# Performance work log

Measured on AMD Instinct MI355X. Metric: run time of the kernel, lower is better.

## Reference

```python
import jax, jax.numpy as jnp
import numpy as np

N, E = 50000, 300000
IN, FC, AC, H, C1, C2, OUT = 1024, 128, 20, 4, 10, 5, 3
FCN = FC + AC + H * C2  # 168


def bn_eval(x, g, b):
    # BatchNorm1d in eval mode with running_mean=0, running_var=1
    return x * (g / jnp.sqrt(1.0 + 1e-5)) + b


def add_self_loops(edge_index, edge_attr, n):
    # PyG add_self_loops with fill_value='mean': self-loop attr = mean of incoming edge attrs
    src, dst = edge_index[0], edge_index[1]
    ones = jnp.ones(src.shape[0], jnp.float32)
    deg = jax.ops.segment_sum(ones, dst, num_segments=n)
    mean_attr = jax.ops.segment_sum(edge_attr, dst, num_segments=n) / jnp.maximum(deg, 1.0)[:, None]
    loop = jnp.arange(n, dtype=src.dtype)
    return (jnp.concatenate([src, loop]), jnp.concatenate([dst, loop]),
            jnp.concatenate([edge_attr, mean_attr], 0))


def gatv2(x, src, dst, eattr, Wl, bl, Wr, br, We, att, b, n):
    # GATv2Conv (concat=True, negative_slope=0.2, edge_dim=1)
    h, c = att.shape
    xl = (x @ Wl + bl).reshape(n, h, c)
    xr = (x @ Wr + br).reshape(n, h, c)
    em = (eattr @ We).reshape(-1, h, c)
    m = jax.nn.leaky_relu(xl[src] + xr[dst] + em, 0.2)   # [E', H, C]
    logit = jnp.einsum('ehc,hc->eh', m, att)              # [E', H]
    mx = jax.ops.segment_max(logit, dst, num_segments=n)
    ex = jnp.exp(logit - mx[dst])
    den = jax.ops.segment_sum(ex, dst, num_segments=n)
    alpha = ex / (den[dst] + 1e-16)                       # segment softmax over dst
    out = jax.ops.segment_sum(xl[src] * alpha[..., None], dst, num_segments=n)
    return out.reshape(n, h * c) + b


def setup_inputs() -> dict:
    key = jax.random.key(0)
    ks = jax.random.split(key, 24)
    rn = lambda k, s: jax.random.normal(k, s, jnp.float32) * 0.05
    return {
        'features': jax.random.normal(ks[0], (N, IN), jnp.float32),
        'edges': jax.random.randint(ks[1], (2, E), 0, N),
        'edges2': jax.random.randint(ks[2], (2, E), 0, N),
        'edge_features': jax.random.normal(ks[3], (E, 1), jnp.float32),
        'additional_features': jax.random.normal(ks[4], (N, AC), jnp.float32),
        'sage_Wl': rn(ks[5], (IN, FC)), 'sage_bl': jnp.zeros((FC,), jnp.float32),
        'sage_Wr': rn(ks[6], (IN, FC)),
        'g1_Wl': rn(ks[7], (AC, H * C1)), 'g1_bl': jnp.zeros((H * C1,), jnp.float32),
        'g1_Wr': rn(ks[8], (AC, H * C1)), 'g1_br': jnp.zeros((H * C1,), jnp.float32),
        'g1_We': rn(ks[9], (1, H * C1)), 'g1_att': rn(ks[10], (H, C1)),
        'g1_b': jnp.zeros((H * C1,), jnp.float32),
        'g2_Wl': rn(ks[11], (H * C1, H * C2)), 'g2_bl': jnp.zeros((H * C2,), jnp.float32),
        'g2_Wr': rn(ks[12], (H * C1, H * C2)), 'g2_br': jnp.zeros((H * C2,), jnp.float32),
        'g2_We': rn(ks[13], (1, H * C2)), 'g2_att': rn(ks[14], (H, C2)),
        'g2_b': jnp.zeros((H * C2,), jnp.float32),
        'fc1_W': rn(ks[15], (FCN, FCN)), 'fc1_b': jnp.zeros((FCN,), jnp.float32),
        'fc2_W': rn(ks[16], (FCN, OUT)), 'fc2_b': jnp.zeros((OUT,), jnp.float32),
        'bnx_g': jnp.ones((FC,), jnp.float32), 'bnx_b': jnp.zeros((FC,), jnp.float32),
        'bny_g': jnp.ones((H * C2,), jnp.float32), 'bny_b': jnp.zeros((H * C2,), jnp.float32),
        'bnf_g': jnp.ones((FCN,), jnp.float32), 'bnf_b': jnp.zeros((FCN,), jnp.float32),
    }


def reference(features, edges, edges2, edge_features, additional_features,
              sage_Wl, sage_bl, sage_Wr,
              g1_Wl, g1_bl, g1_Wr, g1_br, g1_We, g1_att, g1_b,
              g2_Wl, g2_bl, g2_Wr, g2_br, g2_We, g2_att, g2_b,
              fc1_W, fc1_b, fc2_W, fc2_b,
              bnx_g, bnx_b, bny_g, bny_b, bnf_g, bnf_b):
    n = features.shape[0]
    # --- SAGEConv (mean aggr): out = lin_l(mean_j x_j) + lin_r(x_i) ---
    src, dst = edges[0], edges[1]
    deg = jax.ops.segment_sum(jnp.ones(src.shape[0], jnp.float32), dst, num_segments=n)
    aggr = jax.ops.segment_sum(features[src], dst, num_segments=n) / jnp.maximum(deg, 1.0)[:, None]
    x = aggr @ sage_Wl + sage_bl + features @ sage_Wr
    x = bn_eval(x, bnx_g, bnx_b)
    # --- GATv2 stack (self loops with mean edge-attr fill) ---
    s2, d2, ea = add_self_loops(edges2, edge_features, n)
    y = gatv2(additional_features, s2, d2, ea, g1_Wl, g1_bl, g1_Wr, g1_br, g1_We, g1_att, g1_b, n)
    y = jax.nn.leaky_relu(y, 0.01)  # activation (dropout off in eval)
    y = gatv2(y, s2, d2, ea, g2_Wl, g2_bl, g2_Wr, g2_br, g2_We, g2_att, g2_b, n)
    y = bn_eval(y, bny_g, bny_b)
    # --- MLP head ---
    z = jax.nn.leaky_relu(jnp.concatenate([x, y], axis=1), 0.01)
    z = jnp.concatenate([z, additional_features], axis=1) @ fc1_W + fc1_b
    z = jax.nn.relu(bn_eval(z, bnf_g, bnf_b))
    return z @ fc2_W + fc2_b
```

## Files before the change

### kernel.cpp

```cpp
#include <hip/hip_runtime.h>
#include <hip/hip_bf16.h>
#include <cfloat>

__device__ __forceinline__ float lrelu(float x, float a) { return x > 0.0f ? x : a * x; }

__device__ __forceinline__ unsigned short f2bf(float f) {
    unsigned u = __float_as_uint(f);
    unsigned r = (u + 0x7FFFu + ((u >> 16) & 1u)) >> 16;
    return (unsigned short)r;
}
__device__ __forceinline__ float bf2f(unsigned short u) {
    return __uint_as_float((unsigned)u << 16);
}

typedef __attribute__((ext_vector_type(8))) short short8;
typedef __attribute__((ext_vector_type(4))) float f32x4;

#define BN_RSQ 0.99999500003749968750f
#define SCAN_B 256

__global__ void zero_ws(uint4* __restrict__ p, int n16)
{
    int t = blockIdx.x * blockDim.x + threadIdx.x;
    if (t < n16) p[t] = make_uint4(0u, 0u, 0u, 0u);
}

__global__ void prep_all(const float* __restrict__ sWl, const float* __restrict__ sWr,
                         unsigned short* __restrict__ Btp,
                         const float* __restrict__ fc1W, unsigned short* __restrict__ Bt1p,
                         const float* __restrict__ g1Wl, const float* __restrict__ g1Wr,
                         unsigned short* __restrict__ Bg1,
                         const float* __restrict__ g2Wl, const float* __restrict__ g2Wr,
                         unsigned short* __restrict__ Bg2,
                         const int* __restrict__ e1d, const int* __restrict__ e2d,
                         const float* __restrict__ ef,
                         int* __restrict__ cnt1, int* __restrict__ cnt2,
                         float* __restrict__ easum, int E)
{
    int idx = blockIdx.x * blockDim.x + threadIdx.x;
    if (idx < 262144) {
        int j = idx & 7, lane = (idx >> 3) & 63, fn = (idx >> 9) & 3, wid = (idx >> 11) & 3, t = idx >> 13;
        int c = wid * 64 + fn * 16 + (lane & 15);
        int k = t * 32 + (lane >> 4) * 8 + j;
        float v = (c < 128) ? sWl[(size_t)k * 128 + c] : sWr[(size_t)k * 128 + (c - 128)];
        Btp[idx] = f2bf(v);
        return;
    }
    idx -= 262144;
    if (idx < 36864) {
        int j = idx & 7, lane = (idx >> 3) & 63, fn = (idx >> 9) & 3, q = idx >> 11;
        int wid = q % 3, t = q / 3;
        int c = wid * 64 + fn * 16 + (lane & 15);
        int k = t * 32 + (lane >> 4) * 8 + j;
        float v = (c < 168 && k < 168) ? fc1W[(size_t)k * 168 + c] : 0.0f;
        Bt1p[idx] = f2bf(v);
        return;
    }
    idx -= 36864;
    if (idx < 2560) {
        int j = idx & 7, lane = (idx >> 3) & 63, fn = idx >> 9;
        int c = fn * 16 + (lane & 15);
        int k = (lane >> 4) * 8 + j;
        float v = 0.0f;
        if (k < 20) v = (c < 40) ? g1Wl[(size_t)k * 40 + c] : g1Wr[(size_t)k * 40 + (c - 40)];
        Bg1[idx] = f2bf(v);
        return;
    }
    idx -= 2560;
    if (idx < 3072) {
        int j = idx & 7, lane = (idx >> 3) & 63, q = idx >> 9;
        int fn = q % 3, t = q / 3;
        int c = fn * 16 + (lane & 15);
        int k = t * 32 + (lane >> 4) * 8 + j;
        float v = 0.0f;
        if (k < 40 && c < 40) v = (c < 20) ? g2Wl[(size_t)k * 20 + c] : g2Wr[(size_t)k * 20 + (c - 20)];
        Bg2[idx] = f2bf(v);
        return;
    }
    idx -= 3072;
    if (idx < E) {
        atomicAdd(&cnt1[e1d[idx]], 1);
        int d2 = e2d[idx];
        atomicAdd(&cnt2[d2], 1);
        atomicAdd(&easum[d2], ef[idx]);
    }
}

__global__ void scan1(const int* __restrict__ cnt1, const int* __restrict__ cnt2,
                      int* __restrict__ off1, int* __restrict__ off2,
                      int* __restrict__ bsum1, int* __restrict__ bsum2, int M)
{
    __shared__ int sh[SCAN_B];
    int y = blockIdx.y;
    const int* cnt = y ? cnt2 : cnt1;
    int* excl = y ? off2 : off1;
    int* bsum = y ? bsum2 : bsum1;
    int i = blockIdx.x * SCAN_B + threadIdx.x;
    int v = (i < M) ? cnt[i] + y : 0;
    sh[threadIdx.x] = v;
    __syncthreads();
    for (int o = 1; o < SCAN_B; o <<= 1) {
        int t = (threadIdx.x >= o) ? sh[threadIdx.x - o] : 0;
        __syncthreads();
        sh[threadIdx.x] += t;
        __syncthreads();
    }
    if (i < M) excl[i] = sh[threadIdx.x] - v;
    if (threadIdx.x == SCAN_B - 1) bsum[blockIdx.x] = sh[threadIdx.x];
}

__global__ void scan2(int* __restrict__ bsum1, int* __restrict__ bsum2, int nb)
{
    __shared__ int sh[SCAN_B];
    int* bsum = blockIdx.y ? bsum2 : bsum1;
    int v = ((int)threadIdx.x < nb) ? bsum[threadIdx.x] : 0;
    sh[threadIdx.x] = v;
    __syncthreads();
    for (int o = 1; o < SCAN_B; o <<= 1) {
        int t = (threadIdx.x >= o) ? sh[threadIdx.x - o] : 0;
        __syncthreads();
        sh[threadIdx.x] += t;
        __syncthreads();
    }
    if ((int)threadIdx.x < nb) bsum[threadIdx.x] = sh[threadIdx.x] - v;
}

__global__ void scan3(int* __restrict__ off1, int* __restrict__ off2,
                      const int* __restrict__ bsum1, const int* __restrict__ bsum2,
                      const int* __restrict__ cnt1, const int* __restrict__ cnt2,
                      const float* __restrict__ easum, float* __restrict__ ealoop, int M)
{
    int y = blockIdx.y;
    int* off = y ? off2 : off1;
    const int* bsum = y ? bsum2 : bsum1;
    const int* cnt = y ? cnt2 : cnt1;
    int i = blockIdx.x * SCAN_B + threadIdx.x;
    if (i < M) {
        int v = off[i] + bsum[blockIdx.x];
        off[i] = v;
        if (i == M - 1) off[M] = v + cnt[i] + y;
        if (y) ealoop[i] = easum[i] / fmaxf((float)cnt2[i], 1.0f);
    }
}

__global__ __launch_bounds__(256) void stageA(
    const float* __restrict__ A, const unsigned short* __restrict__ Btp,
    unsigned short* __restrict__ P,
    const int* __restrict__ e1s, const int* __restrict__ e1d,
    const int* __restrict__ e2s, const int* __restrict__ e2d,
    const float* __restrict__ ef, const float* __restrict__ ealoop,
    const int* __restrict__ off1, const int* __restrict__ off2,
    int* __restrict__ cnt1, int* __restrict__ cnt2,
    int* __restrict__ srcs1, int2* __restrict__ se2,
    const float* __restrict__ addf, const unsigned short* __restrict__ Bg1,
    const float* __restrict__ g1bl, const float* __restrict__ g1br,
    unsigned short* __restrict__ xl1b, unsigned short* __restrict__ xr1b,
    int M, int E, int Eext, int Gg, int Gf)
{
    __shared__ __align__(16) char smem[20480];
    const int bid = blockIdx.x;
    const int tid = threadIdx.x;

    if (bid < Gg) {
        typedef unsigned short As2_t[64][72];
        As2_t* As2 = reinterpret_cast<As2_t*>(smem);
        const int wid = tid >> 6, lane = tid & 63;
        const int m0 = bid * 64;
        const int l16 = lane & 15, g = lane >> 4;
        const int colbase = wid * 64 + l16;
        const short8* Bv = reinterpret_cast<const short8*>(Btp);
        const int srow = tid >> 4, scol = (tid & 15) * 4;

        f32x4 acc[4][4] = {};
        float4 rcur[4], rnext[4];

#pragma unroll
        for (int p = 0; p < 4; ++p) {
            int ar = m0 + p * 16 + srow;
            rcur[p] = make_float4(0.f, 0.f, 0.f, 0.f);
            if (ar < M) rcur[p] = *reinterpret_cast<const float4*>(&A[(size_t)ar * 1024 + scol]);
        }
#pragma unroll
        for (int p = 0; p < 4; ++p) {
            ushort4 u;
            u.x = f2bf(rcur[p].x); u.y = f2bf(rcur[p].y); u.z = f2bf(rcur[p].z); u.w = f2bf(rcur[p].w);
            *reinterpret_cast<ushort4*>(&As2[0][p * 16 + srow][scol]) = u;
        }
#pragma unroll
        for (int p = 0; p < 4; ++p) {
            int ar = m0 + p * 16 + srow;
            rcur[p] = make_float4(0.f, 0.f, 0.f, 0.f);
            if (ar < M) rcur[p] = *reinterpret_cast<const float4*>(&A[(size_t)ar * 1024 + 64 + scol]);
        }
        __syncthreads();

        for (int c = 0; c < 16; ++c) {
            const int buf = c & 1;
            if (c < 14) {
                const int k0 = (c + 2) * 64;
#pragma unroll
                for (int p = 0; p < 4; ++p) {
                    int ar = m0 + p * 16 + srow;
                    rnext[p] = make_float4(0.f, 0.f, 0.f, 0.f);
                    if (ar < M) rnext[p] = *reinterpret_cast<const float4*>(&A[(size_t)ar * 1024 + k0 + scol]);
                }
            }
#pragma unroll
            for (int t = 0; t < 2; ++t) {
                const int ks = c * 2 + t;
                short8 afr[4], bfr[4];
#pragma unroll
                for (int fm = 0; fm < 4; ++fm)
                    afr[fm] = *reinterpret_cast<const short8*>(&As2[buf][fm * 16 + l16][t * 32 + g * 8]);
#pragma unroll
                for (int fn = 0; fn < 4; ++fn)
                    bfr[fn] = Bv[((ks * 4 + wid) * 4 + fn) * 64 + lane];
#pragma unroll
                for (int fm = 0; fm < 4; ++fm)
#pragma unroll
                    for (int fn = 0; fn < 4; ++fn)
                        acc[fm][fn] = __builtin_amdgcn_mfma_f32_16x16x32_bf16(
                            afr[fm], bfr[fn], acc[fm][fn], 0, 0, 0);
            }
            if (c < 15) {
#pragma unroll
                for (int p = 0; p < 4; ++p) {
                    ushort4 u;
                    u.x = f2bf(rcur[p].x); u.y = f2bf(rcur[p].y);
                    u.z = f2bf(rcur[p].z); u.w = f2bf(rcur[p].w);
                    *reinterpret_cast<ushort4*>(&As2[buf ^ 1][p * 16 + srow][scol]) = u;
                }
            }
            __syncthreads();
#pragma unroll
            for (int p = 0; p < 4; ++p) rcur[p] = rnext[p];
        }

#pragma unroll
        for (int fm = 0; fm < 4; ++fm) {
#pragma unroll
            for (int r = 0; r < 4; ++r) {
                int row = m0 + fm * 16 + g * 4 + r;
                if (row < M) {
#pragma unroll
                    for (int fn = 0; fn < 4; ++fn)
                        P[(size_t)row * 256 + colbase + fn * 16] = f2bf(acc[fm][fn][r]);
                }
            }
        }
    } else if (bid < Gg + Gf) {
        int t = (bid - Gg) * 256 + tid;
        if (t < E) {
            int d = e1d[t];
            int pos = atomicSub(&cnt1[d], 1) - 1;
            srcs1[off1[d] + pos] = e1s[t];
        }
        int t2 = t - E;
        if (t2 >= 0 && t2 < Eext) {
            if (t2 < E) {
                int d = e2d[t2];
                int pos = atomicSub(&cnt2[d], 1) - 1;
                se2[off2[d] + pos] = make_int2(e2s[t2], __float_as_int(ef[t2]));
            } else {
                int nn = t2 - E;
                se2[off2[nn + 1] - 1] = make_int2(nn, __float_as_int(ealoop[nn]));
            }
        }
    } else {
        const int wid = tid >> 6, lane = tid & 63;
        const int tile = (bid - Gg - Gf) * 4 + wid;
        const int m0 = tile * 64;
        if (m0 >= M) return;
        unsigned short (*xs)[40] = reinterpret_cast<unsigned short(*)[40]>(smem + wid * 5120);
        const int l16 = lane & 15, g = lane >> 4;
        const short8* Bv = reinterpret_cast<const short8*>(Bg1);

#pragma unroll
        for (int i = 0; i < 5; ++i) {
            int q = i * 64 + lane;
            int f = q * 4;
            int row = f / 20, col = f % 20;
            int ar = m0 + row;
            float4 v = make_float4(0.f, 0.f, 0.f, 0.f);
            if (ar < M) v = *reinterpret_cast<const float4*>(&addf[(size_t)ar * 20 + col]);
            ushort4 u;
            u.x = f2bf(v.x); u.y = f2bf(v.y); u.z = f2bf(v.z); u.w = f2bf(v.w);
            *reinterpret_cast<ushort4*>(&xs[row][col]) = u;
        }
        ushort4 zz; zz.x = 0; zz.y = 0; zz.z = 0; zz.w = 0;
#pragma unroll
        for (int c = 20; c < 32; c += 4)
            *reinterpret_cast<ushort4*>(&xs[lane][c]) = zz;

        f32x4 acc[4][5] = {};
        short8 afr[4], bfr[5];
#pragma unroll
        for (int fm = 0; fm < 4; ++fm)
            afr[fm] = *reinterpret_cast<const short8*>(&xs[fm * 16 + l16][g * 8]);
#pragma unroll
        for (int fn = 0; fn < 5; ++fn)
            bfr[fn] = Bv[fn * 64 + lane];
#pragma unroll
        for (int fm = 0; fm < 4; ++fm)
#pragma unroll
            for (int fn = 0; fn < 5; ++fn)
                acc[fm][fn] = __builtin_amdgcn_mfma_f32_16x16x32_bf16(
                    afr[fm], bfr[fn], acc[fm][fn], 0, 0, 0);

#pragma unroll
        for (int fm = 0; fm < 4; ++fm) {
#pragma unroll
            for (int r = 0; r < 4; ++r) {
                int row = m0 + fm * 16 + g * 4 + r;
                if (row < M) {
#pragma unroll
                    for (int fn = 0; fn < 5; ++fn) {
                        int col = fn * 16 + l16;
                        float v = acc[fm][fn][r];
                        if (col < 40) {
                            int h = col / 10, c = col % 10;
                            xl1b[((size_t)row * 4 + h) * 16 + c] = f2bf(v + g1bl[col]);
                        } else if (col < 80) {
                            int cc = col - 40, h = cc / 10, c = cc % 10;
                            xr1b[((size_t)row * 4 + h) * 16 + c] = f2bf(v + g1br[cc]);
                        }
                    }
                }
            }
        }
    }
}

template <int H, int C, int BPAD, int MODE>
__device__ __forceinline__ void gat_node_core(
    const int2* __restrict__ se2, const int* __restrict__ off2,
    const unsigned short* __restrict__ xlb, const unsigned short* __restrict__ xrb,
    const float* __restrict__ We, const float* __restrict__ att,
    const float* __restrict__ b,
    const float* __restrict__ bng, const float* __restrict__ bnb,
    void* __restrict__ outv, int n, int h)
{
    float xrc[C], atth[C], weh[C];
    {
        short8 sv[BPAD / 8];
#pragma unroll
        for (int q = 0; q < BPAD / 8; ++q)
            sv[q] = *reinterpret_cast<const short8*>(&xrb[((size_t)n * H + h) * BPAD + q * 8]);
#pragma unroll
        for (int c = 0; c < C; ++c) xrc[c] = bf2f((unsigned short)sv[c / 8][c % 8]);
    }
#pragma unroll
    for (int c = 0; c < C; ++c) {
        atth[c] = att[h * C + c];
        weh[c]  = We[h * C + c];
    }

    const int beg = off2[n], end = off2[n + 1];
    float mx = -FLT_MAX, den = 0.0f;
    float accv[C] = {};
    for (int j = beg; j < end; ++j) {
        int2 se = se2[j];
        int s = se.x;
        float ea = __int_as_float(se.y);
        short8 sv[BPAD / 8];
#pragma unroll
        for (int q = 0; q < BPAD / 8; ++q)
            sv[q] = *reinterpret_cast<const short8*>(&xlb[((size_t)s * H + h) * BPAD + q * 8]);
        float xv[C];
        float lg = 0.0f;
#pragma unroll
        for (int c = 0; c < C; ++c) {
            xv[c] = bf2f((unsigned short)sv[c / 8][c % 8]);
            float m = xv[c] + xrc[c] + ea * weh[c];
            lg += lrelu(m, 0.2f) * atth[c];
        }
        if (lg > mx) {
            float sc = __expf(mx - lg);
            den *= sc;
#pragma unroll
            for (int c = 0; c < C; ++c) accv[c] *= sc;
            mx = lg;
        }
        float ex = __expf(lg - mx);
        den += ex;
#pragma unroll
        for (int c = 0; c < C; ++c) accv[c] += ex * xv[c];
    }
    float inv = 1.0f / (den + 1e-16f);

#pragma unroll
    for (int c = 0; c < C; ++c) {
        int jch = h * C + c;
        float v = accv[c] * inv + b[jch];
        if (MODE == 1) {
            ((float*)outv)[(size_t)n * (H * C) + jch] = lrelu(v, 0.01f);
        } else {
            v = v * (bng[jch] * BN_RSQ) + bnb[jch];
            ((unsigned short*)outv)[(size_t)n * 168 + 128 + jch] = f2bf(lrelu(v, 0.01f));
        }
    }
}

__global__ void stageB(const int* __restrict__ srcs1, const int* __restrict__ off1,
                       const unsigned short* __restrict__ P, const float* __restrict__ bl,
                       const float* __restrict__ bng, const float* __restrict__ bnb,
                       unsigned short* __restrict__ z,
                       const int2* __restrict__ se2, const int* __restrict__ off2,
                       const unsigned short* __restrict__ xl1b, const unsigned short* __restrict__ xr1b,
                       const float* __restrict__ g1We, const float* __restrict__ g1att,
                       const float* __restrict__ g1b, float* __restrict__ y1,
                       int N, int Gg)
{
    const int bid = blockIdx.x;
    if (bid < Gg) {
        int t = bid * 256 + threadIdx.x;
        if (t >= N * 16) return;
        int n = t >> 4, g = t & 15;
        int beg = off1[n], end = off1[n + 1];
        float a[8] = {};
        for (int j = beg; j < end; ++j) {
            int s = srcs1[j];
            short8 v = *reinterpret_cast<const short8*>(&P[(size_t)s * 256 + g * 8]);
#pragma unroll
            for (int k = 0; k < 8; ++k) a[k] += bf2f((unsigned short)v[k]);
        }
        float inv = 1.0f / fmaxf((float)(end - beg), 1.0f);
        short8 pr = *reinterpret_cast<const short8*>(&P[(size_t)n * 256 + 128 + g * 8]);
        short8 zo;
#pragma unroll
        for (int k = 0; k < 8; ++k) {
            int cc = g * 8 + k;
            float x = a[k] * inv + bl[cc] + bf2f((unsigned short)pr[k]);
            x = x * (bng[cc] * BN_RSQ) + bnb[cc];
            zo[k] = (short)f2bf(lrelu(x, 0.01f));
        }
        *reinterpret_cast<short8*>(&z[(size_t)n * 168 + g * 8]) = zo;
    } else {
        int t = (bid - Gg) * 256 + threadIdx.x;
        if (t >= N * 4) return;
        gat_node_core<4, 10, 16, 1>(se2, off2, xl1b, xr1b, g1We, g1att, g1b,
                                    nullptr, nullptr, (void*)y1, t >> 2, t & 3);
    }
}

__global__ __launch_bounds__(64) void gat_lin2_mfma(
    const float* __restrict__ X, const unsigned short* __restrict__ Bp,
    const float* __restrict__ bl, const float* __restrict__ br,
    unsigned short* __restrict__ xlb, unsigned short* __restrict__ xrb, int M)
{
    __shared__ unsigned short xs[64][72];
    const int lane = threadIdx.x;
    const int m0 = blockIdx.x * 64;
    const int l16 = lane & 15, g = lane >> 4;
    const short8* Bv = reinterpret_cast<const short8*>(Bp);

#pragma unroll
    for (int i = 0; i < 10; ++i) {
        int q = i * 64 + lane;
        int f = q * 4;
        int row = f / 40, col = f % 40;
        int ar = m0 + row;
        float4 v = make_float4(0.f, 0.f, 0.f, 0.f);
        if (ar < M) v = *reinterpret_cast<const float4*>(&X[(size_t)ar * 40 + col]);
        ushort4 u;
        u.x = f2bf(v.x); u.y = f2bf(v.y); u.z = f2bf(v.z); u.w = f2bf(v.w);
        *reinterpret_cast<ushort4*>(&xs[row][col]) = u;
    }
    ushort4 zz; zz.x = 0; zz.y = 0; zz.z = 0; zz.w = 0;
#pragma unroll
    for (int c = 40; c < 64; c += 4)
        *reinterpret_cast<ushort4*>(&xs[lane][c]) = zz;

    f32x4 acc[4][3] = {};
#pragma unroll
    for (int t = 0; t < 2; ++t) {
        short8 afr[4], bfr[3];
#pragma unroll
        for (int fm = 0; fm < 4; ++fm)
            afr[fm] = *reinterpret_cast<const short8*>(&xs[fm * 16 + l16][t * 32 + g * 8]);
#pragma unroll
        for (int fn = 0; fn < 3; ++fn)
            bfr[fn] = Bv[(t * 3 + fn) * 64 + lane];
#pragma unroll
        for (int fm = 0; fm < 4; ++fm)
#pragma unroll
            for (int fn = 0; fn < 3; ++fn)
                acc[fm][fn] = __builtin_amdgcn_mfma_f32_16x16x32_bf16(
                    afr[fm], bfr[fn], acc[fm][fn], 0, 0, 0);
    }

#pragma unroll
    for (int fm = 0; fm < 4; ++fm) {
#pragma unroll
        for (int r = 0; r < 4; ++r) {
            int row = m0 + fm * 16 + g * 4 + r;
            if (row < M) {
#pragma unroll
                for (int fn = 0; fn < 3; ++fn) {
                    int col = fn * 16 + l16;
                    float v = acc[fm][fn][r];
                    if (col < 20) {
                        int h = col / 5, c = col % 5;
                        xlb[((size_t)row * 4 + h) * 8 + c] = f2bf(v + bl[col]);
                    } else if (col < 40) {
                        int cc = col - 20, h = cc / 5, c = cc % 5;
                        xrb[((size_t)row * 4 + h) * 8 + c] = f2bf(v + br[cc]);
                    }
                }
            }
        }
    }
}

__global__ void gat_node2(const int2* __restrict__ se2, const int* __restrict__ off2,
                          const unsigned short* __restrict__ xlb, const unsigned short* __restrict__ xrb,
                          const float* __restrict__ We, const float* __restrict__ att,
                          const float* __restrict__ b,
                          const float* __restrict__ bng, const float* __restrict__ bnb,
                          unsigned short* __restrict__ z, int N)
{
    int t = blockIdx.x * blockDim.x + threadIdx.x;
    if (t >= N * 4) return;
    gat_node_core<4, 5, 8, 2>(se2, off2, xlb, xrb, We, att, b, bng, bnb, (void*)z, t >> 2, t & 3);
}

__global__ __launch_bounds__(256) void mlp_mfma(
    const unsigned short* __restrict__ z, const float* __restrict__ addf,
    const unsigned short* __restrict__ Bt1p,
    const float* __restrict__ fc1b, const float* __restrict__ bnfg, const float* __restrict__ bnfb,
    const float* __restrict__ fc2W, const float* __restrict__ fc2b,
    float* __restrict__ out, int M)
{
    __shared__ __align__(16) char smem[64 * 169 * 4];
    unsigned short (*zs)[200] = reinterpret_cast<unsigned short(*)[200]>(smem);
    float (*ts)[169] = reinterpret_cast<float(*)[169]>(smem);
    const int tid = threadIdx.x;
    const int wid = tid >> 6, lane = tid & 63;
    const int m0 = blockIdx.x * 64;
    const int l16 = lane & 15, g = lane >> 4;
    const short8* Bv = reinterpret_cast<const short8*>(Bt1p);

#pragma unroll
    for (int p = 0; p < 13; ++p) {
        int idx = p * 256 + tid;
        if (idx < 3200) {
            int row = idx / 50, c4 = (idx % 50) * 4;
            int ar = m0 + row;
            ushort4 u; u.x = 0; u.y = 0; u.z = 0; u.w = 0;
            if (ar < M) {
                if (c4 < 148) {
                    u = *reinterpret_cast<const ushort4*>(&z[(size_t)ar * 168 + c4]);
                } else if (c4 < 168) {
                    float4 v = *reinterpret_cast<const float4*>(&addf[(size_t)ar * 20 + (c4 - 148)]);
                    u.x = f2bf(v.x); u.y = f2bf(v.y); u.z = f2bf(v.z); u.w = f2bf(v.w);
                }
            }
            *reinterpret_cast<ushort4*>(&zs[row][c4]) = u;
        }
    }
    __syncthreads();

    f32x4 acc[4][4] = {};
    if (wid < 3) {
#pragma unroll
        for (int t = 0; t < 6; ++t) {
            short8 afr[4], bfr[4];
#pragma unroll
            for (int fm = 0; fm < 4; ++fm)
                afr[fm] = *reinterpret_cast<const short8*>(&zs[fm * 16 + l16][t * 32 + g * 8]);
#pragma unroll
            for (int fn = 0; fn < 4; ++fn)
                bfr[fn] = Bv[((t * 3 + wid) * 4 + fn) * 64 + lane];
#pragma unroll
            for (int fm = 0; fm < 4; ++fm)
#pragma unroll
                for (int fn = 0; fn < 4; ++fn)
                    acc[fm][fn] = __builtin_amdgcn_mfma_f32_16x16x32_bf16(
                        afr[fm], bfr[fn], acc[fm][fn], 0, 0, 0);
        }
    }
    __syncthreads();
    if (wid < 3) {
        const int colbase = wid * 64 + l16;
#pragma unroll
        for (int fm = 0; fm < 4; ++fm) {
#pragma unroll
            for (int r = 0; r < 4; ++r) {
                int rr = fm * 16 + g * 4 + r;
#pragma unroll
                for (int fn = 0; fn < 4; ++fn) {
                    int col = colbase + fn * 16;
                    if (col < 168) {
                        float v = acc[fm][fn][r] + fc1b[col];
                        v = v * (bnfg[col] * BN_RSQ) + bnfb[col];
                        ts[rr][col] = fmaxf(v, 0.0f);
                    }
                }
            }
        }
    }
    __syncthreads();
    if (tid < 192) {
        int r = tid & 63, c = tid >> 6;
        float acc2 = fc2b[c];
#pragma unroll 4
        for (int k = 0; k < 168; ++k) acc2 += ts[r][k] * fc2W[k * 3 + c];
        int row = m0 + r;
        if (row < M) out[(size_t)row * 3 + c] = acc2;
    }
}

extern "C" void kernel_launch(void* const* d_in, const int* in_sizes, int n_in,
                              void* d_out, int out_size, void* d_ws, size_t ws_size,
                              hipStream_t stream)
{
    const float* features = (const float*)d_in[0];
    const int*   e1       = (const int*)d_in[1];
    const int*   e2       = (const int*)d_in[2];
    const float* ef       = (const float*)d_in[3];
    const float* addf     = (const float*)d_in[4];
    const float* sage_Wl  = (const float*)d_in[5];
    const float* sage_bl  = (const float*)d_in[6];
    const float* sage_Wr  = (const float*)d_in[7];
    const float* g1_Wl = (const float*)d_in[8];
    const float* g1_bl = (const float*)d_in[9];
    const float* g1_Wr = (const float*)d_in[10];
    const float* g1_br = (const float*)d_in[11];
    const float* g1_We = (const float*)d_in[12];
    const float* g1_att = (const float*)d_in[13];
    const float* g1_b = (const float*)d_in[14];
    const float* g2_Wl = (const float*)d_in[15];
    const float* g2_bl = (const float*)d_in[16];
    const float* g2_Wr = (const float*)d_in[17];
    const float* g2_br = (const float*)d_in[18];
    const float* g2_We = (const float*)d_in[19];
    const float* g2_att = (const float*)d_in[20];
    const float* g2_b = (const float*)d_in[21];
    const float* fc1_W = (const float*)d_in[22];
    const float* fc1_b = (const float*)d_in[23];
    const float* fc2_W = (const float*)d_in[24];
    const float* fc2_b = (const float*)d_in[25];
    const float* bnx_g = (const float*)d_in[26];
    const float* bnx_b = (const float*)d_in[27];
    const float* bny_g = (const float*)d_in[28];
    const float* bny_b = (const float*)d_in[29];
    const float* bnf_g = (const float*)d_in[30];
    const float* bnf_b = (const float*)d_in[31];

    const int N = in_sizes[0] / 1024;
    const int E = in_sizes[3];
    const int Eext = E + N;
    const int* e1s = e1, *e1d = e1 + E;
    const int* e2s = e2, *e2d = e2 + E;
    const int nb = (N + SCAN_B - 1) / SCAN_B;

    char* wb = (char*)d_ws;
    size_t off = 0;
    auto takeB = [&](size_t bytes) { char* p = wb + off; off = (off + bytes + 255) & ~(size_t)255; return p; };
    unsigned short* P = (unsigned short*)takeB((size_t)N * 256 * 2);
    unsigned short* z = (unsigned short*)takeB((size_t)N * 168 * 2);
    float* ealoop = (float*)takeB((size_t)N * 4);
    unsigned short* xl1b = (unsigned short*)takeB((size_t)N * 64 * 2);
    unsigned short* xr1b = (unsigned short*)takeB((size_t)N * 64 * 2);
    float* y1 = (float*)takeB((size_t)N * 40 * 4);
    unsigned short* xl2b = (unsigned short*)takeB((size_t)N * 32 * 2);
    unsigned short* xr2b = (unsigned short*)takeB((size_t)N * 32 * 2);
    unsigned short* Btp  = (unsigned short*)takeB((size_t)256 * 1024 * 2);
    unsigned short* Bt1p = (unsigned short*)takeB((size_t)36864 * 2);
    unsigned short* Bg1  = (unsigned short*)takeB((size_t)2560 * 2);
    unsigned short* Bg2  = (unsigned short*)takeB((size_t)3072 * 2);
    char* zero_beg = wb + off;
    int* cnt1    = (int*)takeB((size_t)N * 4);
    int* cnt2    = (int*)takeB((size_t)N * 4);
    float* easum = (float*)takeB((size_t)N * 4);
    size_t zero_len = (size_t)((wb + off) - zero_beg);
    int* off1  = (int*)takeB((size_t)(N + 1) * 4);
    int* off2  = (int*)takeB((size_t)(N + 1) * 4);
    int* bsum1 = (int*)takeB(SCAN_B * 4);
    int* bsum2 = (int*)takeB(SCAN_B * 4);
    int* srcs1 = (int*)takeB((size_t)E * 4);
    int2* se2  = (int2*)takeB((size_t)Eext * 8);

    const int B = 256;
    const int n16 = (int)(zero_len / 16);
    zero_ws<<<(n16 + B - 1) / B, B, 0, stream>>>((uint4*)zero_beg, n16);

    const int prep_total = 262144 + 36864 + 2560 + 3072 + E;
    prep_all<<<(prep_total + B - 1) / B, B, 0, stream>>>(
        sage_Wl, sage_Wr, Btp, fc1_W, Bt1p,
        g1_Wl, g1_Wr, Bg1, g2_Wl, g2_Wr, Bg2,
        e1d, e2d, ef, cnt1, cnt2, easum, E);

    scan1<<<dim3(nb, 2), SCAN_B, 0, stream>>>(cnt1, cnt2, off1, off2, bsum1, bsum2, N);
    scan2<<<dim3(1, 2), SCAN_B, 0, stream>>>(bsum1, bsum2, nb);
    scan3<<<dim3(nb, 2), SCAN_B, 0, stream>>>(off1, off2, bsum1, bsum2, cnt1, cnt2,
                                              easum, ealoop, N);

    const int mtiles = (N + 63) / 64;
    const int Gf = (E + Eext + B - 1) / B;
    const int Gl = (mtiles + 3) / 4;
    stageA<<<mtiles + Gf + Gl, 256, 0, stream>>>(
        features, Btp, P,
        e1s, e1d, e2s, e2d, ef, ealoop, off1, off2, cnt1, cnt2, srcs1, se2,
        addf, Bg1, g1_bl, g1_br, xl1b, xr1b,
        N, E, Eext, mtiles, Gf);

    const int Gg = (N * 16 + B - 1) / B;
    const int Gn = (N * 4 + B - 1) / B;
    stageB<<<Gg + Gn, 256, 0, stream>>>(
        srcs1, off1, P, sage_bl, bnx_g, bnx_b, z,
        se2, off2, xl1b, xr1b, g1_We, g1_att, g1_b, y1, N, Gg);

    gat_lin2_mfma<<<mtiles, 64, 0, stream>>>(y1, Bg2, g2_bl, g2_br, xl2b, xr2b, N);
    gat_node2<<<Gn, 256, 0, stream>>>(se2, off2, xl2b, xr2b, g2_We, g2_att, g2_b,
                                      bny_g, bny_b, z, N);

    mlp_mfma<<<mtiles, 256, 0, stream>>>(z, addf, Bt1p, fc1_b, bnf_g, bnf_b, fc2_W, fc2_b,
                                         (float*)d_out, N);
}
```

Baseline: 260.6 us.

## Fuse second GAT node aggregation into MLP kernel and hoist B-fragment loads

The second GATv2 per-node softmax aggregation now runs inside the MLP kernel and writes its 20 output channels straight into shared memory, so the separate gat_node2 launch and its z round-trip are gone and z shrinks to 128 columns. The SAGE GEMM loads both k-step B fragments at the top of each chunk, ahead of the next A-tile global loads, and replaces __syncthreads with an lgkmcnt-only wait plus barrier. This saves one launch and global traffic, but the MLP blocks now carry an irregular edge loop (256 threads per 64 rows), which may add imbalance and register pressure.

After: 258.8 us. No clear change (-0.7%).

```diff
diff --git a/kernel.cpp b/kernel.cpp
--- a/kernel.cpp
+++ b/kernel.cpp
@@ -18,6 +18,7 @@
 
 #define BN_RSQ 0.99999500003749968750f
 #define SCAN_B 256
+#define BAR_LGKM() asm volatile("s_waitcnt lgkmcnt(0)\n\ts_barrier" ::: "memory")
 
 __global__ void zero_ws(uint4* __restrict__ p, int n16)
 {
@@ -192,10 +193,16 @@
             rcur[p] = make_float4(0.f, 0.f, 0.f, 0.f);
             if (ar < M) rcur[p] = *reinterpret_cast<const float4*>(&A[(size_t)ar * 1024 + 64 + scol]);
         }
-        __syncthreads();
+        BAR_LGKM();
 
         for (int c = 0; c < 16; ++c) {
             const int buf = c & 1;
+            short8 bfr[2][4];
+#pragma unroll
+            for (int t = 0; t < 2; ++t)
+#pragma unroll
+                for (int fn = 0; fn < 4; ++fn)
+                    bfr[t][fn] = Bv[(((c * 2 + t) * 4 + wid) * 4 + fn) * 64 + lane];
             if (c < 14) {
                 const int k0 = (c + 2) * 64;
 #pragma unroll
@@ -207,20 +214,16 @@
             }
 #pragma unroll
             for (int t = 0; t < 2; ++t) {
-                const int ks = c * 2 + t;
-                short8 afr[4], bfr[4];
+                short8 afr[4];
 #pragma unroll
                 for (int fm = 0; fm < 4; ++fm)
                     afr[fm] = *reinterpret_cast<const short8*>(&As2[buf][fm * 16 + l16][t * 32 + g * 8]);
 #pragma unroll
-                for (int fn = 0; fn < 4; ++fn)
-                    bfr[fn] = Bv[((ks * 4 + wid) * 4 + fn) * 64 + lane];
-#pragma unroll
                 for (int fm = 0; fm < 4; ++fm)
 #pragma unroll
                     for (int fn = 0; fn < 4; ++fn)
                         acc[fm][fn] = __builtin_amdgcn_mfma_f32_16x16x32_bf16(
-                            afr[fm], bfr[fn], acc[fm][fn], 0, 0, 0);
+                            afr[fm], bfr[t][fn], acc[fm][fn], 0, 0, 0);
             }
             if (c < 15) {
 #pragma unroll
@@ -231,7 +234,7 @@
                     *reinterpret_cast<ushort4*>(&As2[buf ^ 1][p * 16 + srow][scol]) = u;
                 }
             }
-            __syncthreads();
+            BAR_LGKM();
 #pragma unroll
             for (int p = 0; p < 4; ++p) rcur[p] = rnext[p];
         }
@@ -331,14 +334,12 @@
     }
 }
 
-template <int H, int C, int BPAD, int MODE>
-__device__ __forceinline__ void gat_node_core(
+template <int H, int C, int BPAD>
+__device__ __forceinline__ void gat_node_compute(
     const int2* __restrict__ se2, const int* __restrict__ off2,
     const unsigned short* __restrict__ xlb, const unsigned short* __restrict__ xrb,
     const float* __restrict__ We, const float* __restrict__ att,
-    const float* __restrict__ b,
-    const float* __restrict__ bng, const float* __restrict__ bnb,
-    void* __restrict__ outv, int n, int h)
+    int n, int h, float* __restrict__ outc)
 {
     float xrc[C], atth[C], weh[C];
     {
@@ -387,24 +388,14 @@
         for (int c = 0; c < C; ++c) accv[c] += ex * xv[c];
     }
     float inv = 1.0f / (den + 1e-16f);
-
-#pragma unroll
-    for (int c = 0; c < C; ++c) {
-        int jch = h * C + c;
-        float v = accv[c] * inv + b[jch];
-        if (MODE == 1) {
-            ((float*)outv)[(size_t)n * (H * C) + jch] = lrelu(v, 0.01f);
-        } else {
-            v = v * (bng[jch] * BN_RSQ) + bnb[jch];
-            ((unsigned short*)outv)[(size_t)n * 168 + 128 + jch] = f2bf(lrelu(v, 0.01f));
-        }
-    }
+#pragma unroll
+    for (int c = 0; c < C; ++c) outc[c] = accv[c] * inv;
 }
 
 __global__ void stageB(const int* __restrict__ srcs1, const int* __restrict__ off1,
                        const unsigned short* __restrict__ P, const float* __restrict__ bl,
                        const float* __restrict__ bng, const float* __restrict__ bnb,
-                       unsigned short* __restrict__ z,
+                       unsigned short* __restrict__ z128,
                        const int2* __restrict__ se2, const int* __restrict__ off2,
                        const unsigned short* __restrict__ xl1b, const unsigned short* __restrict__ xr1b,
                        const float* __restrict__ g1We, const float* __restrict__ g1att,
@@ -434,12 +425,18 @@
             x = x * (bng[cc] * BN_RSQ) + bnb[cc];
             zo[k] = (short)f2bf(lrelu(x, 0.01f));
         }
-        *reinterpret_cast<short8*>(&z[(size_t)n * 168 + g * 8]) = zo;
+        *reinterpret_cast<short8*>(&z128[(size_t)n * 128 + g * 8]) = zo;
     } else {
         int t = (bid - Gg) * 256 + threadIdx.x;
         if (t >= N * 4) return;
-        gat_node_core<4, 10, 16, 1>(se2, off2, xl1b, xr1b, g1We, g1att, g1b,
-                                    nullptr, nullptr, (void*)y1, t >> 2, t & 3);
+        int n = t >> 2, h = t & 3;
+        float oc[10];
+        gat_node_compute<4, 10, 16>(se2, off2, xl1b, xr1b, g1We, g1att, n, h, oc);
+#pragma unroll
+        for (int c = 0; c < 10; ++c) {
+            int jch = h * 10 + c;
+            y1[(size_t)n * 40 + jch] = lrelu(oc[c] + g1b[jch], 0.01f);
+        }
     }
 }
 
@@ -512,20 +509,13 @@
     }
 }
 
-__global__ void gat_node2(const int2* __restrict__ se2, const int* __restrict__ off2,
-                          const unsigned short* __restrict__ xlb, const unsigned short* __restrict__ xrb,
-                          const float* __restrict__ We, const float* __restrict__ att,
-                          const float* __restrict__ b,
-                          const float* __restrict__ bng, const float* __restrict__ bnb,
-                          unsigned short* __restrict__ z, int N)
-{
-    int t = blockIdx.x * blockDim.x + threadIdx.x;
-    if (t >= N * 4) return;
-    gat_node_core<4, 5, 8, 2>(se2, off2, xlb, xrb, We, att, b, bng, bnb, (void*)z, t >> 2, t & 3);
-}
-
 __global__ __launch_bounds__(256) void mlp_mfma(
-    const unsigned short* __restrict__ z, const float* __restrict__ addf,
+    const unsigned short* __restrict__ z128, const float* __restrict__ addf,
+    const int2* __restrict__ se2, const int* __restrict__ off2,
+    const unsigned short* __restrict__ xl2b, const unsigned short* __restrict__ xr2b,
+    const float* __restrict__ g2We, const float* __restrict__ g2att,
+    const float* __restrict__ g2b,
+    const float* __restrict__ bnyg, const float* __restrict__ bnyb,
     const unsigned short* __restrict__ Bt1p,
     const float* __restrict__ fc1b, const float* __restrict__ bnfg, const float* __restrict__ bnfb,
     const float* __restrict__ fc2W, const float* __restrict__ fc2b,
@@ -540,17 +530,37 @@
     const int l16 = lane & 15, g = lane >> 4;
     const short8* Bv = reinterpret_cast<const short8*>(Bt1p);
 
+    {
+        int row = tid >> 2, h = tid & 3;
+        int n = m0 + row;
+        if (n < M) {
+            float oc[5];
+            gat_node_compute<4, 5, 8>(se2, off2, xl2b, xr2b, g2We, g2att, n, h, oc);
+#pragma unroll
+            for (int c = 0; c < 5; ++c) {
+                int jch = h * 5 + c;
+                float v = oc[c] + g2b[jch];
+                v = v * (bnyg[jch] * BN_RSQ) + bnyb[jch];
+                zs[row][128 + jch] = f2bf(lrelu(v, 0.01f));
+            }
+        } else {
+#pragma unroll
+            for (int c = 0; c < 5; ++c) zs[row][128 + h * 5 + c] = 0;
+        }
+    }
+
 #pragma unroll
     for (int p = 0; p < 13; ++p) {
         int idx = p * 256 + tid;
         if (idx < 3200) {
             int row = idx / 50, c4 = (idx % 50) * 4;
+            if (c4 >= 128 && c4 < 148) continue;
             int ar = m0 + row;
             ushort4 u; u.x = 0; u.y = 0; u.z = 0; u.w = 0;
             if (ar < M) {
-                if (c4 < 148) {
-                    u = *reinterpret_cast<const ushort4*>(&z[(size_t)ar * 168 + c4]);
-                } else if (c4 < 168) {
+                if (c4 < 128) {
+                    u = *reinterpret_cast<const ushort4*>(&z128[(size_t)ar * 128 + c4]);
+                } else if (c4 >= 148 && c4 < 168) {
                     float4 v = *reinterpret_cast<const float4*>(&addf[(size_t)ar * 20 + (c4 - 148)]);
                     u.x = f2bf(v.x); u.y = f2bf(v.y); u.z = f2bf(v.z); u.w = f2bf(v.w);
                 }
@@ -658,7 +668,7 @@
     size_t off = 0;
     auto takeB = [&](size_t bytes) { char* p = wb + off; off = (off + bytes + 255) & ~(size_t)255; return p; };
     unsigned short* P = (unsigned short*)takeB((size_t)N * 256 * 2);
-    unsigned short* z = (unsigned short*)takeB((size_t)N * 168 * 2);
+    unsigned short* z128 = (unsigned short*)takeB((size_t)N * 128 * 2);
     float* ealoop = (float*)takeB((size_t)N * 4);
     unsigned short* xl1b = (unsigned short*)takeB((size_t)N * 64 * 2);
     unsigned short* xr1b = (unsigned short*)takeB((size_t)N * 64 * 2);
@@ -708,13 +718,12 @@
     const int Gg = (N * 16 + B - 1) / B;
     const int Gn = (N * 4 + B - 1) / B;
     stageB<<<Gg + Gn, 256, 0, stream>>>(
-        srcs1, off1, P, sage_bl, bnx_g, bnx_b, z,
+        srcs1, off1, P, sage_bl, bnx_g, bnx_b, z128,
         se2, off2, xl1b, xr1b, g1_We, g1_att, g1_b, y1, N, Gg);
 
     gat_lin2_mfma<<<mtiles, 64, 0, stream>>>(y1, Bg2, g2_bl, g2_br, xl2b, xr2b, N);
-    gat_node2<<<Gn, 256, 0, stream>>>(se2, off2, xl2b, xr2b, g2_We, g2_att, g2_b,
-                                      bny_g, bny_b, z, N);
-
-    mlp_mfma<<<mtiles, 256, 0, stream>>>(z, addf, Bt1p, fc1_b, bnf_g, bnf_b, fc2_W, fc2_b,
-                                         (float*)d_out, N);
-}
+
+    mlp_mfma<<<mtiles, 256, 0, stream>>>(
+        z128, addf, se2, off2, xl2b, xr2b, g2_We, g2_att, g2_b, bny_g, bny_b,
+        Bt1p, fc1_b, bnf_g, bnf_b, fc2_W, fc2_b, (float*)d_out, N);
+}
```
